# Performance work log

Hardware: AMD Instinct MI355X
Metric: run time of the kernel (lower is better)

Reference implementation:

```python
import jax, jax.numpy as jnp
import numpy as np

EPS = 1e-12  # F.normalize eps

def _unfold3(x):
    # x: [B,C,H,W] -> [B, C*9, H*W], matching F.unfold(kernel=3, padding=1)
    B, C, H, W = x.shape
    xp = jnp.pad(x, ((0, 0), (0, 0), (1, 1), (1, 1)))
    pats = jnp.stack([xp[:, :, i:i + H, j:j + W]
                      for i in range(3) for j in range(3)], axis=2)  # [B,C,9,H,W]
    return pats.reshape(B, C * 9, H * W)

def _fold3(t, H, W):
    # inverse of _unfold3 with overlap-add, matching F.fold(kernel=3, padding=1)
    B, CK, L = t.shape
    C = CK // 9
    t = t.reshape(B, C, 3, 3, H, W)
    out = jnp.zeros((B, C, H + 2, W + 2), t.dtype)
    for i in range(3):
        for j in range(3):
            out = out.at[:, :, i:i + H, j:j + W].add(t[:, :, i, j])
    return out[:, :, 1:1 + H, 1:1 + W]

def setup_inputs() -> dict:
    key = jax.random.key(0)
    kV, kK, kQ = jax.random.split(key, 3)
    B, C, H, W = 4, 64, 64, 64
    return {
        'V': jax.random.normal(kV, (B, C, H, W), dtype=jnp.float32),
        'K': jax.random.normal(kK, (B, C, H, W), dtype=jnp.float32),
        'Q': jax.random.normal(kQ, (B, C, H, W), dtype=jnp.float32),
    }

def reference(V, K, Q):
    B, C, H, W = Q.shape
    Qu = _unfold3(Q)  # [B, C9, L]
    Ku = _unfold3(K)  # [B, C9, L]
    # F.normalize along the feature (C*9) axis for both K (after permute dim=2) and Q (dim=1)
    Kn = Ku / jnp.maximum(jnp.linalg.norm(Ku, axis=1, keepdims=True), EPS)
    Qn = Qu / jnp.maximum(jnp.linalg.norm(Qu, axis=1, keepdims=True), EPS)
    # R[b,k,q] = <Kn[b,:,k], Qn[b,:,q]>  -> [B, L, L]
    R = jnp.einsum('bfk,bfq->bkq', Kn, Qn)
    S = jnp.max(R, axis=1)        # [B, L]
    arg = jnp.argmax(R, axis=1)   # [B, L] best key patch per query position
    Vu = _unfold3(V)              # [B, C9, L]
    idx = jnp.broadcast_to(arg[:, None, :], Vu.shape)
    T_unfold = jnp.take_along_axis(Vu, idx, axis=2)  # gather along patch dim
    T = _fold3(T_unfold, H, W) / 9.0                 # [B, C, H, W]
    S = S.reshape(B, 1, H, W)
    return (S, T)
```

## Files before the change

kernel.cpp:

```cpp
#include <hip/hip_runtime.h>
#include <math.h>

#define HW 4096

typedef short bf16x8 __attribute__((ext_vector_type(8)));
typedef float floatx4 __attribute__((ext_vector_type(4)));
typedef unsigned short u16x8 __attribute__((ext_vector_type(8)));

__device__ __forceinline__ unsigned short f2bf_rne(float x) {
    unsigned int u = __float_as_uint(x);
    unsigned int r = (u + 0x7FFFu + ((u >> 16) & 1u)) >> 16;
    return (unsigned short)r;
}
__device__ __forceinline__ float bf2f(unsigned short h) {
    return __uint_as_float(((unsigned int)h) << 16);
}

__device__ __forceinline__ void gload_lds16(const void* gptr, void* lptr) {
    auto g = (const __attribute__((address_space(1))) unsigned int*)(unsigned long long)(gptr);
    auto l = (__attribute__((address_space(3))) unsigned int*)(unsigned int)(unsigned long long)(lptr);
    __builtin_amdgcn_global_load_lds(g, l, 16, 0, 0);
}

__global__ __launch_bounds__(256)
void prep_kernel(const float* __restrict__ Q, const float* __restrict__ K,
                 const float* __restrict__ V,
                 unsigned short* __restrict__ Aq, unsigned short* __restrict__ Bq,
                 float* __restrict__ VT,
                 float* __restrict__ pix2q, float* __restrict__ pix2k) {
    __shared__ float sT[64][65];
    const int tid = threadIdx.x;
    const int p0 = blockIdx.x * 64;
    const int b = blockIdx.y;
    const int which = blockIdx.z;
    const float* __restrict__ src = (which == 0) ? Q : ((which == 1) ? K : V);

#pragma unroll
    for (int it = 0; it < 16; ++it) {
        int idx = it * 256 + tid;
        int c = idx >> 6, x = idx & 63;
        sT[c][x] = src[((size_t)b * 64 + c) * HW + p0 + x];
    }
    __syncthreads();
    const int pp = tid >> 2, qt = tid & 3;

    if (which == 2) {
        float* dst = VT + ((size_t)b * 4096 + p0 + pp) * 64 + qt * 16;
#pragma unroll
        for (int j = 0; j < 4; ++j) {
            float4 v = make_float4(sT[qt * 16 + 4 * j + 0][pp], sT[qt * 16 + 4 * j + 1][pp],
                                   sT[qt * 16 + 4 * j + 2][pp], sT[qt * 16 + 4 * j + 3][pp]);
            *(float4*)(dst + 4 * j) = v;
        }
        return;
    }

    const int isK = which;
    unsigned short* __restrict__ dst = isK ? Bq : Aq;
    float* __restrict__ pix2 = isK ? pix2k : pix2q;
    const size_t base = ((size_t)b * 4096 + p0 + pp) * 192;
    {
        float sq = 0.f;
        u16x8 hv[2], lv[2];
#pragma unroll
        for (int g = 0; g < 2; ++g)
#pragma unroll
            for (int j = 0; j < 8; ++j) {
                int c = qt * 16 + g * 8 + j;
                float x = sT[c][pp];
                sq = fmaf(x, x, sq);
                unsigned short h = f2bf_rne(x);
                hv[g][j] = h;
                lv[g][j] = f2bf_rne(x - bf2f(h));
            }
        sq += __shfl_xor(sq, 1, 64);
        sq += __shfl_xor(sq, 2, 64);
        if (qt == 0) pix2[(b << 12) + p0 + pp] = sq;
#pragma unroll
        for (int g = 0; g < 2; ++g) {
            int co = qt * 16 + g * 8;
            *(u16x8*)(dst + base + co)       = hv[g];
            *(u16x8*)(dst + base + 64 + co)  = isK ? lv[g] : hv[g];
            *(u16x8*)(dst + base + 128 + co) = isK ? hv[g] : lv[g];
        }
    }
}

__global__ void patchnorm_kernel(const float* __restrict__ pix2q, const float* __restrict__ pix2k,
                                 float* __restrict__ rnq, float* __restrict__ rnk) {
    int idx = blockIdx.x * 256 + threadIdx.x;
    int b = idx >> 12, p = idx & 4095;
    int py = p >> 6, px = p & 63;
    float sq = 0.f, sk = 0.f;
    for (int dy = -1; dy <= 1; ++dy)
        for (int dx = -1; dx <= 1; ++dx) {
            int yy = py + dy, xx = px + dx;
            if ((unsigned)yy < 64u && (unsigned)xx < 64u) {
                int o = (b << 12) + (yy << 6) + xx;
                sq += pix2q[o];
                sk += pix2k[o];
            }
        }
    rnq[idx] = 1.f / fmaxf(sqrtf(sq), 1e-12f);
    rnk[idx] = 1.f / fmaxf(sqrtf(sk), 1e-12f);
}

#define WAITV(n_) asm volatile("s_waitcnt vmcnt(" #n_ ")" ::: "memory")
#define PBAR(n_) do { WAITV(n_); __builtin_amdgcn_s_barrier(); \
                      asm volatile("" ::: "memory"); } while (0)

#define ISSUE_A(c_, sg_, slot_) do { \
    const char* g_ = Aqb + (size_t)(q0 - 64 + (c_) * 64) * 384 + (sg_) * 128; \
    gload_lds16(g_ + g0off, smem + (slot_) * 8192 + l0off); \
    gload_lds16(g_ + g1off, smem + (slot_) * 8192 + l1off); \
} while (0)
#define ISSUE_B(c_, sg_, slot_) do { \
    const char* g_ = Bqb + (size_t)(k0 - 64 + (c_) * 64) * 384 + (sg_) * 128; \
    gload_lds16(g_ + g0off, smemB + (slot_) * 8192 + l0off); \
    gload_lds16(g_ + g1off, smemB + (slot_) * 8192 + l1off); \
} while (0)

#define MM16(af_, bfr_) do { \
    __builtin_amdgcn_s_setprio(1); \
    _Pragma("unroll") \
    for (int mt = 0; mt < 4; ++mt) \
        _Pragma("unroll") \
        for (int nt = 0; nt < 4; ++nt) \
            acc[mt][nt] = __builtin_amdgcn_mfma_f32_16x16x32_bf16( \
                (af_)[mt], (bfr_)[nt], acc[mt][nt], 0, 0, 0); \
    __builtin_amdgcn_s_setprio(0); \
} while (0)

#define STEP_S0(D_) do { \
    const char* As_ = smem + (wm + (D_)) * 8192; \
    const char* Bs_ = smemB + (wn + (D_)) * 8192; \
    _Pragma("unroll") \
    for (int kk = 0; kk < 2; ++kk) { \
        const int pk_ = kk ? posK1 : posK0; \
        _Pragma("unroll") \
        for (int mt = 0; mt < 4; ++mt) \
            afc[kk][mt] = *(const bf16x8*)(As_ + mt * 2048 + rowB + pk_); \
        _Pragma("unroll") \
        for (int nt = 0; nt < 4; ++nt) \
            bfc[kk][nt] = *(const bf16x8*)(Bs_ + nt * 2048 + rowB + pk_); \
        MM16(afc[kk], bfc[kk]); \
    } \
} while (0)

#define STEP_S1(D_) do { \
    const int xb_ = wn + (D_); \
    const char* Bs_ = smemB + (xb_ < 2 ? xb_ + 3 : xb_ - 2) * 8192; \
    _Pragma("unroll") \
    for (int kk = 0; kk < 2; ++kk) { \
        const int pk_ = kk ? posK1 : posK0; \
        bf16x8 bfr[4]; \
        _Pragma("unroll") \
        for (int nt = 0; nt < 4; ++nt) \
            bfr[nt] = *(const bf16x8*)(Bs_ + nt * 2048 + rowB + pk_); \
        MM16(afc[kk], bfr); \
    } \
} while (0)

#define STEP_S2(D_) do { \
    const int xa_ = wm + (D_); \
    const char* As_ = smem + ((xa_ & 1) ? (xa_ >> 1) : 4) * 8192; \
    _Pragma("unroll") \
    for (int kk = 0; kk < 2; ++kk) { \
        const int pk_ = kk ? posK1 : posK0; \
        bf16x8 af[4]; \
        _Pragma("unroll") \
        for (int mt = 0; mt < 4; ++mt) \
            af[mt] = *(const bf16x8*)(As_ + mt * 2048 + rowB + pk_); \
        MM16(af, bfc[kk]); \
    } \
} while (0)

__global__ __launch_bounds__(256, 2)
void gemm_fused_kernel(const unsigned short* __restrict__ Aq, const unsigned short* __restrict__ Bq,
                       const float* __restrict__ rnkA,
                       float* __restrict__ part_val, int* __restrict__ part_arg) {
    __shared__ __align__(16) char smem[81920];
    char* const smemB = smem + 40960;
    const int tid = threadIdx.x;
    const int lane = tid & 63, wid = tid >> 6;
    const int m15 = lane & 15, quad = lane >> 4;
    const int wm = wid & 1, wn = wid >> 1;
    const int f = blockIdx.x + (blockIdx.y << 5);
    const int o = ((f & 7) << 7) + (f >> 3);
    const int kt = o & 31, qt = o >> 5;
    const int k0 = kt << 7;
    const int q0 = qt << 7;
    const int b = blockIdx.z;
    const char* Aqb = (const char*)(Aq + (size_t)b * 4096 * 192);
    const char* Bqb = (const char*)(Bq + (size_t)b * 4096 * 192);
    const bool aInt = (q0 >= 64) && (q0 <= 4096 - 192);
    const bool bInt = (k0 >= 64) && (k0 <= 4096 - 192);

    const int rr0 = tid >> 3, ps = tid & 7;
    const int g0off = rr0 * 384 + (ps ^ (rr0 & 7)) * 16;
    const int l0off = tid * 16;
    const int rr1 = (256 + tid) >> 3;
    const int g1off = rr1 * 384 + (ps ^ (rr1 & 7)) * 16;
    const int l1off = (256 + tid) * 16;
    const int rowB = m15 * 128;
    const int posK0 = (quad ^ (m15 & 7)) * 16;
    const int posK1 = ((4 + quad) ^ (m15 & 7)) * 16;

    floatx4 acc[4][4];
#pragma unroll
    for (int i = 0; i < 4; ++i)
#pragma unroll
        for (int j = 0; j < 4; ++j) acc[i][j] = (floatx4)0.f;

    bf16x8 afc[2][4];
    bf16x8 bfc[2][4];

    if (aInt && bInt) {
        ISSUE_A(0, 0, 0); ISSUE_A(1, 0, 1); ISSUE_B(0, 0, 0); ISSUE_B(1, 0, 1);
        ISSUE_A(2, 0, 2); ISSUE_B(2, 0, 2); ISSUE_A(3, 0, 3); ISSUE_B(0, 1, 3);
        ISSUE_B(1, 1, 4); ISSUE_A(0, 2, 4);
        PBAR(12);                                      STEP_S0(0);
        PBAR(2);  ISSUE_A(1, 2, 0); ISSUE_B(2, 1, 0); STEP_S1(0);
        PBAR(2);  ISSUE_B(3, 0, 3);                   STEP_S2(0);
        PBAR(14); ISSUE_A(2, 2, 4);                   STEP_S0(1);
        PBAR(4);  ISSUE_B(3, 1, 1);                   STEP_S1(1);
        PBAR(2);  ISSUE_A(3, 2, 1);                   STEP_S2(1);
        PBAR(6);                                      STEP_S0(2);
        PBAR(2);                                      STEP_S1(2);
        PBAR(0);                                      STEP_S2(2);
        __syncthreads();
    } else {
        for (int seg = 0; seg < 3; ++seg) {
            const char* abL = Aqb + (size_t)(q0 - 64) * 384 + seg * 128;
            const char* bbL = Bqb + (size_t)(k0 - 64) * 384 + seg * 128;
            if (aInt) {
#pragma unroll
                for (int it = 0; it < 8; ++it) {
                    int slot = it * 256 + tid;
                    int row = slot >> 3, pos = slot & 7;
                    int G = pos ^ (row & 7);
                    gload_lds16(abL + (size_t)row * 384 + G * 16, smem + slot * 16);
                }
            } else {
#pragma unroll
                for (int it = 0; it < 8; ++it) {
                    int slot = it * 256 + tid;
                    int row = slot >> 3, pos = slot & 7;
                    int G = pos ^ (row & 7);
                    uint4 v = make_uint4(0u, 0u, 0u, 0u);
                    if ((unsigned)(q0 - 64 + row) < 4096u)
                        v = *(const uint4*)(abL + (size_t)row * 384 + G * 16);
                    *(uint4*)(smem + slot * 16) = v;
                }
            }
            if (bInt) {
#pragma unroll
                for (int it = 0; it < 8; ++it) {
                    int slot = it * 256 + tid;
                    int row = slot >> 3, pos = slot & 7;
                    int G = pos ^ (row & 7);
                    gload_lds16(bbL + (size_t)row * 384 + G * 16, smemB + slot * 16);
                }
            } else {
#pragma unroll
                for (int it = 0; it < 8; ++it) {
                    int slot = it * 256 + tid;
                    int row = slot >> 3, pos = slot & 7;
                    int G = pos ^ (row & 7);
                    uint4 v = make_uint4(0u, 0u, 0u, 0u);
                    if ((unsigned)(k0 - 64 + row) < 4096u)
                        v = *(const uint4*)(bbL + (size_t)row * 384 + G * 16);
                    *(uint4*)(smemB + slot * 16) = v;
                }
            }
            __syncthreads();
            STEP_S0(0); STEP_S0(1); STEP_S0(2);
            __syncthreads();
        }
    }

    float* Csh = (float*)smem;
    float* bvs = (float*)(smem + 34816);
    int*   bas = (int*)(smem + 35840);
    const int q_l = tid & 63;
    const int qr = tid >> 6;
    const int c0 = qr * 32;
    const float4 zero4 = make_float4(0.f, 0.f, 0.f, 0.f);

#pragma unroll
    for (int h = 0; h < 2; ++h) {
        if (h) __syncthreads();
        if (wm == h) {
#pragma unroll
            for (int mt = 0; mt < 4; ++mt)
#pragma unroll
                for (int nt = 0; nt < 4; ++nt)
#pragma unroll
                    for (int j = 0; j < 4; ++j)
                        Csh[(mt * 16 + quad * 4 + j) * 133 + wn * 64 + nt * 16 + m15] =
                            acc[mt][nt][j];
        }
        __syncthreads();

        const bool qm = q_l > 0;
        const bool qp = q_l < 63;
        const float* rC = Csh + q_l * 133;
        const float* rM = Csh + (q_l - 1) * 133;
        const float* rP = Csh + (q_l + 1) * 133;
        float4 prevm = (qm && c0 > 0) ? *(const float4*)&rM[c0 - 4] : zero4;
        float4 rpj   = qp ? *(const float4*)&rP[c0] : zero4;
        float bv = -INFINITY;
        int ba = 0;
#pragma unroll
        for (int j = 0; j < 8; ++j) {
            int c = c0 + 4 * j;
            float4 cen = *(const float4*)&rC[c];
            float4 rm4 = qm ? *(const float4*)&rM[c] : zero4;
            float4 rp1 = (qp && (c + 4) < 128) ? *(const float4*)&rP[c + 4] : zero4;
            float4 o4;
            o4.x = cen.x + (((c & 63) != 0) ? prevm.w : 0.f) + rpj.y;
            o4.y = cen.y + rm4.x + rpj.z;
            o4.z = cen.z + rm4.y + rpj.w;
            o4.w = cen.w + rm4.z + ((((c + 3) & 63) != 63) ? rp1.x : 0.f);
            float4 rk = *(const float4*)&rnkA[(b << 12) + k0 + c];
            float v0 = o4.x * rk.x; if (v0 > bv) { bv = v0; ba = k0 + c + 0; }
            float v1 = o4.y * rk.y; if (v1 > bv) { bv = v1; ba = k0 + c + 1; }
            float v2 = o4.z * rk.z; if (v2 > bv) { bv = v2; ba = k0 + c + 2; }
            float v3 = o4.w * rk.w; if (v3 > bv) { bv = v3; ba = k0 + c + 3; }
            prevm = rm4;
            rpj = rp1;
        }
        bvs[(qr << 6) + q_l] = bv;
        bas[(qr << 6) + q_l] = ba;
        __syncthreads();
        if (tid < 64) {
            float v = bvs[tid];
            int a = bas[tid];
#pragma unroll
            for (int s = 1; s < 4; ++s) {
                float v2 = bvs[(s << 6) + tid];
                if (v2 > v) { v = v2; a = bas[(s << 6) + tid]; }
            }
            int q = q0 + h * 64 + tid;
            part_val[(((b << 5) + kt) << 12) + q] = v;
            part_arg[(((b << 5) + kt) << 12) + q] = a;
        }
    }
}

__global__ __launch_bounds__(256)
void argcombine_kernel(const float* __restrict__ part_val, const int* __restrict__ part_arg,
                       const float* __restrict__ rnqA,
                       float* __restrict__ S_out, int* __restrict__ argF) {
    __shared__ float rv[4][64];
    __shared__ int ra[4][64];
    const int tid = threadIdx.x;
    const int qi = tid & 63, sg = tid >> 6;
    const int q = blockIdx.x * 64 + qi;
    const int b = blockIdx.y;
    const int base = (b << 17) + q;
    float bv = -INFINITY; int ba = 0;
#pragma unroll
    for (int s8 = 0; s8 < 8; ++s8) {
        int s = sg * 8 + s8;
        float v = part_val[base + (s << 12)];
        int aa = part_arg[base + (s << 12)];
        if (v > bv) { bv = v; ba = aa; }
    }
    rv[sg][qi] = bv; ra[sg][qi] = ba;
    __syncthreads();
    if (tid < 64) {
        float v = rv[0][tid]; int a = ra[0][tid];
#pragma unroll
        for (int s = 1; s < 4; ++s) {
            float v2 = rv[s][tid];
            if (v2 > v) { v = v2; a = ra[s][tid]; }
        }
        int idx = (b << 12) + blockIdx.x * 64 + tid;
        S_out[idx] = v * rnqA[idx];
        argF[idx] = a;
    }
}

__global__ __launch_bounds__(256)
void gatherT_kernel(const float* __restrict__ VT, const int* __restrict__ argF,
                    float* __restrict__ T_out) {
    __shared__ int sArg[192];
    const int y = blockIdx.x, b = blockIdx.y, cg = blockIdx.z;
    const int tid = threadIdx.x;
    if (tid < 192) {
        int r = tid >> 6, x = tid & 63;
        int yy = y - 1 + r;
        sArg[tid] = ((unsigned)yy < 64u) ? argF[(b << 12) + (yy << 6) + x] : 0;
    }
    __syncthreads();

    const int x = tid >> 2, cq = tid & 3;
    const float* Vb = VT + (size_t)b * 4096 * 64 + cg * 16 + cq * 4;
    float ax = 0.f, ay = 0.f, az = 0.f, aw = 0.f;
#pragma unroll
    for (int t = 0; t < 9; ++t) {
        int dy = t / 3 - 1, dx = t % 3 - 1;
        int qy = y - dy, qx = x - dx;
        if ((unsigned)qy < 64u && (unsigned)qx < 64u) {
            int a = sArg[(1 - dy) * 64 + qx];
            int sy = (a >> 6) + dy, sx = (a & 63) + dx;
            if ((unsigned)sy < 64u && (unsigned)sx < 64u) {
                float4 v = *(const float4*)(Vb + (size_t)((sy << 6) + sx) * 64);
                ax += v.x; ay += v.y; az += v.z; aw += v.w;
            }
        }
    }
    float* Tb = T_out + ((size_t)b * 64 + cg * 16 + cq * 4) * HW + (y << 6) + x;
    Tb[0]          = ax * (1.f / 9.f);
    Tb[HW]         = ay * (1.f / 9.f);
    Tb[2 * HW]     = az * (1.f / 9.f);
    Tb[3 * HW]     = aw * (1.f / 9.f);
}

extern "C" void kernel_launch(void* const* d_in, const int* in_sizes, int n_in,
                              void* d_out, int out_size, void* d_ws, size_t ws_size,
                              hipStream_t stream) {
    const float* V = (const float*)d_in[0];
    const float* K = (const float*)d_in[1];
    const float* Q = (const float*)d_in[2];
    float* S_out = (float*)d_out;
    float* T_out = S_out + 4 * HW;

    char* ws = (char*)d_ws;
    float* pix2q = (float*)(ws + 0);
    float* pix2k = (float*)(ws + 65536);
    float* rnq   = (float*)(ws + 131072);
    float* rnk   = (float*)(ws + 196608);
    float* part_val = (float*)(ws + 262144);
    int*   argF  = (int*)(ws + 4456448);
    int*   part_arg = (int*)(ws + 8650752);
    float* VT    = (float*)(ws + 10747904);
    unsigned short* Aq = (unsigned short*)(ws + 17039360);
    unsigned short* Bq = (unsigned short*)(ws + 23330816);

    prep_kernel<<<dim3(64, 4, 3), 256, 0, stream>>>(Q, K, V, Aq, Bq, VT, pix2q, pix2k);
    patchnorm_kernel<<<64, 256, 0, stream>>>(pix2q, pix2k, rnq, rnk);
    gemm_fused_kernel<<<dim3(32, 32, 4), 256, 0, stream>>>(Aq, Bq, rnk, part_val, part_arg);
    argcombine_kernel<<<dim3(64, 4), 256, 0, stream>>>(part_val, part_arg, rnq, S_out, argF);
    gatherT_kernel<<<dim3(64, 4, 4), 256, 0, stream>>>(VT, argF, T_out);
}
```

Measured before the change: 191.8 us.

## Enlarge GEMM tile to 256x256 with 512 threads and split hi/lo operand buffers

The fused correlation GEMM now computes 256x256 output tiles per block with 8 waves, each holding a 128x64 accumulator. The prep kernel stores the hi and lo bf16 parts in separate places, and the GEMM loads them into distinct LDS regions through a 5-slot ring. Each dy step issues three MFMA passes (hi*hi, hi*lo, lo*hi). The larger tiles raise data reuse per loaded byte and halve the number of partial argmax results that argcombine has to merge. In exchange the kernel uses 160KB of LDS with one block per CU, carries more accumulator register pressure, and has a simpler pipeline with less overlap.

```diff
diff --git a/kernel.cpp b/kernel.cpp
--- a/kernel.cpp
+++ b/kernel.cpp
@@ -79,9 +79,8 @@
 #pragma unroll
         for (int g = 0; g < 2; ++g) {
             int co = qt * 16 + g * 8;
-            *(u16x8*)(dst + base + co)       = hv[g];
-            *(u16x8*)(dst + base + 64 + co)  = isK ? lv[g] : hv[g];
-            *(u16x8*)(dst + base + 128 + co) = isK ? hv[g] : lv[g];
+            *(u16x8*)(dst + base + co)                     = hv[g];
+            *(u16x8*)(dst + base + (isK ? 64 : 128) + co)  = lv[g];
         }
     }
 }
@@ -106,207 +105,169 @@
 }
 
 #define WAITV(n_) asm volatile("s_waitcnt vmcnt(" #n_ ")" ::: "memory")
-#define PBAR(n_) do { WAITV(n_); __builtin_amdgcn_s_barrier(); \
-                      asm volatile("" ::: "memory"); } while (0)
-
-#define ISSUE_A(c_, sg_, slot_) do { \
-    const char* g_ = Aqb + (size_t)(q0 - 64 + (c_) * 64) * 384 + (sg_) * 128; \
-    gload_lds16(g_ + g0off, smem + (slot_) * 8192 + l0off); \
-    gload_lds16(g_ + g1off, smem + (slot_) * 8192 + l1off); \
+#define SB do { __builtin_amdgcn_s_barrier(); asm volatile("" ::: "memory"); } while (0)
+
+#define AHB 0
+#define ALB 40960
+#define BHB 81920
+#define BLB 122880
+#define SLOT5(u_) ((u_) >= 5 ? (u_) - 5 : (u_))
+
+#define ISS4(c_) do { \
+    const size_t ro_ = (size_t)((c_) * 64 + rr) * 384; \
+    gload_lds16(agb + ro_ +   0 + G16, smem + AHB + ((c_) % 5) * 8192 + t16); \
+    gload_lds16(agb + ro_ + 256 + G16, smem + ALB + ((c_) % 5) * 8192 + t16); \
+    gload_lds16(bgb + ro_ +   0 + G16, smem + BHB + ((c_) % 5) * 8192 + t16); \
+    gload_lds16(bgb + ro_ + 128 + G16, smem + BLB + ((c_) % 5) * 8192 + t16); \
 } while (0)
-#define ISSUE_B(c_, sg_, slot_) do { \
-    const char* g_ = Bqb + (size_t)(k0 - 64 + (c_) * 64) * 384 + (sg_) * 128; \
-    gload_lds16(g_ + g0off, smemB + (slot_) * 8192 + l0off); \
-    gload_lds16(g_ + g1off, smemB + (slot_) * 8192 + l1off); \
+
+#define GISS4(c_) do { \
+    const size_t ro_ = (size_t)((c_) * 64 + rr) * 384; \
+    uint4 va_ = make_uint4(0u,0u,0u,0u), vl_ = va_, wh_ = va_, wl_ = va_; \
+    if ((unsigned)(arow + (c_) * 64 + rr) < 4096u) { \
+        va_ = *(const uint4*)(agb + ro_ + G16); \
+        vl_ = *(const uint4*)(agb + ro_ + 256 + G16); } \
+    if ((unsigned)(brow + (c_) * 64 + rr) < 4096u) { \
+        wh_ = *(const uint4*)(bgb + ro_ + G16); \
+        wl_ = *(const uint4*)(bgb + ro_ + 128 + G16); } \
+    *(uint4*)(smem + AHB + ((c_) % 5) * 8192 + t16) = va_; \
+    *(uint4*)(smem + ALB + ((c_) % 5) * 8192 + t16) = vl_; \
+    *(uint4*)(smem + BHB + ((c_) % 5) * 8192 + t16) = wh_; \
+    *(uint4*)(smem + BLB + ((c_) % 5) * 8192 + t16) = wl_; \
 } while (0)
 
-#define MM16(af_, bfr_) do { \
+#define MM32(af_, bf_) do { \
     __builtin_amdgcn_s_setprio(1); \
     _Pragma("unroll") \
-    for (int mt = 0; mt < 4; ++mt) \
+    for (int mt_ = 0; mt_ < 8; ++mt_) \
         _Pragma("unroll") \
-        for (int nt = 0; nt < 4; ++nt) \
-            acc[mt][nt] = __builtin_amdgcn_mfma_f32_16x16x32_bf16( \
-                (af_)[mt], (bfr_)[nt], acc[mt][nt], 0, 0, 0); \
+        for (int nt_ = 0; nt_ < 4; ++nt_) \
+            acc[mt_][nt_] = __builtin_amdgcn_mfma_f32_16x16x32_bf16( \
+                (af_)[mt_], (bf_)[nt_], acc[mt_][nt_], 0, 0, 0); \
     __builtin_amdgcn_s_setprio(0); \
 } while (0)
 
-#define STEP_S0(D_) do { \
-    const char* As_ = smem + (wm + (D_)) * 8192; \
-    const char* Bs_ = smemB + (wn + (D_)) * 8192; \
+#define DY_STEP(dy_) do { \
+    const int sa0_ = SLOT5(wm2 * 2 + (dy_)); \
+    const int sa1_ = SLOT5(wm2 * 2 + (dy_) + 1); \
+    const int sb_  = SLOT5(wn + (dy_)); \
+    const char* Ah0_ = smem + AHB + sa0_ * 8192 + m15 * 128; \
+    const char* Ah1_ = smem + AHB + sa1_ * 8192 + m15 * 128; \
+    const char* Al0_ = smem + ALB + sa0_ * 8192 + m15 * 128; \
+    const char* Al1_ = smem + ALB + sa1_ * 8192 + m15 * 128; \
+    const char* Bh_  = smem + BHB + sb_ * 8192 + m15 * 128; \
+    const char* Bl_  = smem + BLB + sb_ * 8192 + m15 * 128; \
     _Pragma("unroll") \
     for (int kk = 0; kk < 2; ++kk) { \
         const int pk_ = kk ? posK1 : posK0; \
+        bf16x8 afc[8], bfc[4], tf[8]; \
         _Pragma("unroll") \
-        for (int mt = 0; mt < 4; ++mt) \
-            afc[kk][mt] = *(const bf16x8*)(As_ + mt * 2048 + rowB + pk_); \
+        for (int mt = 0; mt < 8; ++mt) \
+            afc[mt] = *(const bf16x8*)((mt < 4 ? Ah0_ : Ah1_) + (mt & 3) * 2048 + pk_); \
         _Pragma("unroll") \
         for (int nt = 0; nt < 4; ++nt) \
-            bfc[kk][nt] = *(const bf16x8*)(Bs_ + nt * 2048 + rowB + pk_); \
-        MM16(afc[kk], bfc[kk]); \
+            bfc[nt] = *(const bf16x8*)(Bh_ + nt * 2048 + pk_); \
+        MM32(afc, bfc); \
+        _Pragma("unroll") \
+        for (int nt = 0; nt < 4; ++nt) \
+            tf[nt] = *(const bf16x8*)(Bl_ + nt * 2048 + pk_); \
+        MM32(afc, tf); \
+        _Pragma("unroll") \
+        for (int mt = 0; mt < 8; ++mt) \
+            tf[mt] = *(const bf16x8*)((mt < 4 ? Al0_ : Al1_) + (mt & 3) * 2048 + pk_); \
+        MM32(tf, bfc); \
     } \
 } while (0)
 
-#define STEP_S1(D_) do { \
-    const int xb_ = wn + (D_); \
-    const char* Bs_ = smemB + (xb_ < 2 ? xb_ + 3 : xb_ - 2) * 8192; \
-    _Pragma("unroll") \
-    for (int kk = 0; kk < 2; ++kk) { \
-        const int pk_ = kk ? posK1 : posK0; \
-        bf16x8 bfr[4]; \
-        _Pragma("unroll") \
-        for (int nt = 0; nt < 4; ++nt) \
-            bfr[nt] = *(const bf16x8*)(Bs_ + nt * 2048 + rowB + pk_); \
-        MM16(afc[kk], bfr); \
-    } \
-} while (0)
-
-#define STEP_S2(D_) do { \
-    const int xa_ = wm + (D_); \
-    const char* As_ = smem + ((xa_ & 1) ? (xa_ >> 1) : 4) * 8192; \
-    _Pragma("unroll") \
-    for (int kk = 0; kk < 2; ++kk) { \
-        const int pk_ = kk ? posK1 : posK0; \
-        bf16x8 af[4]; \
-        _Pragma("unroll") \
-        for (int mt = 0; mt < 4; ++mt) \
-            af[mt] = *(const bf16x8*)(As_ + mt * 2048 + rowB + pk_); \
-        MM16(af, bfc[kk]); \
-    } \
-} while (0)
-
-__global__ __launch_bounds__(256, 2)
+__global__ __launch_bounds__(512, 1)
 void gemm_fused_kernel(const unsigned short* __restrict__ Aq, const unsigned short* __restrict__ Bq,
                        const float* __restrict__ rnkA,
                        float* __restrict__ part_val, int* __restrict__ part_arg) {
-    __shared__ __align__(16) char smem[81920];
-    char* const smemB = smem + 40960;
+    __shared__ __align__(16) char smem[163840];
     const int tid = threadIdx.x;
     const int lane = tid & 63, wid = tid >> 6;
     const int m15 = lane & 15, quad = lane >> 4;
-    const int wm = wid & 1, wn = wid >> 1;
-    const int f = blockIdx.x + (blockIdx.y << 5);
-    const int o = ((f & 7) << 7) + (f >> 3);
-    const int kt = o & 31, qt = o >> 5;
-    const int k0 = kt << 7;
-    const int q0 = qt << 7;
-    const int b = blockIdx.z;
-    const char* Aqb = (const char*)(Aq + (size_t)b * 4096 * 192);
-    const char* Bqb = (const char*)(Bq + (size_t)b * 4096 * 192);
-    const bool aInt = (q0 >= 64) && (q0 <= 4096 - 192);
-    const bool bInt = (k0 >= 64) && (k0 <= 4096 - 192);
-
-    const int rr0 = tid >> 3, ps = tid & 7;
-    const int g0off = rr0 * 384 + (ps ^ (rr0 & 7)) * 16;
-    const int l0off = tid * 16;
-    const int rr1 = (256 + tid) >> 3;
-    const int g1off = rr1 * 384 + (ps ^ (rr1 & 7)) * 16;
-    const int l1off = (256 + tid) * 16;
-    const int rowB = m15 * 128;
+    const int wn = wid & 3, wm2 = wid >> 2;
+    const int f = blockIdx.x;
+    const int o = ((f & 7) << 5) + (f >> 3);
+    const int kt = o & 15, qt = o >> 4;
+    const int k0 = kt << 8, q0 = qt << 8;
+    const int b = blockIdx.y;
+    const int arow = q0 - 64, brow = k0 - 64;
+    const char* agb = (const char*)(Aq + (size_t)b * 4096 * 192) + (ptrdiff_t)arow * 384;
+    const char* bgb = (const char*)(Bq + (size_t)b * 4096 * 192) + (ptrdiff_t)brow * 384;
+    const bool aInt = (q0 >= 64) && (q0 + 320 <= 4096);
+    const bool bInt = (k0 >= 64) && (k0 + 320 <= 4096);
+
+    const int rr = tid >> 3;
+    const int G16 = ((tid & 7) ^ (rr & 7)) * 16;
+    const int t16 = tid * 16;
     const int posK0 = (quad ^ (m15 & 7)) * 16;
     const int posK1 = ((4 + quad) ^ (m15 & 7)) * 16;
 
-    floatx4 acc[4][4];
-#pragma unroll
-    for (int i = 0; i < 4; ++i)
+    floatx4 acc[8][4];
+#pragma unroll
+    for (int i = 0; i < 8; ++i)
 #pragma unroll
         for (int j = 0; j < 4; ++j) acc[i][j] = (floatx4)0.f;
 
-    bf16x8 afc[2][4];
-    bf16x8 bfc[2][4];
-
     if (aInt && bInt) {
-        ISSUE_A(0, 0, 0); ISSUE_A(1, 0, 1); ISSUE_B(0, 0, 0); ISSUE_B(1, 0, 1);
-        ISSUE_A(2, 0, 2); ISSUE_B(2, 0, 2); ISSUE_A(3, 0, 3); ISSUE_B(0, 1, 3);
-        ISSUE_B(1, 1, 4); ISSUE_A(0, 2, 4);
-        PBAR(12);                                      STEP_S0(0);
-        PBAR(2);  ISSUE_A(1, 2, 0); ISSUE_B(2, 1, 0); STEP_S1(0);
-        PBAR(2);  ISSUE_B(3, 0, 3);                   STEP_S2(0);
-        PBAR(14); ISSUE_A(2, 2, 4);                   STEP_S0(1);
-        PBAR(4);  ISSUE_B(3, 1, 1);                   STEP_S1(1);
-        PBAR(2);  ISSUE_A(3, 2, 1);                   STEP_S2(1);
-        PBAR(6);                                      STEP_S0(2);
-        PBAR(2);                                      STEP_S1(2);
-        PBAR(0);                                      STEP_S2(2);
+        ISS4(0); ISS4(1); ISS4(2); ISS4(3);
+        ISS4(4);
+        WAITV(4); SB;
+        DY_STEP(0);
+        SB;
+        ISS4(5);
+        WAITV(4); SB;
+        DY_STEP(1);
+        SB; WAITV(0); SB;
+        DY_STEP(2);
         __syncthreads();
     } else {
-        for (int seg = 0; seg < 3; ++seg) {
-            const char* abL = Aqb + (size_t)(q0 - 64) * 384 + seg * 128;
-            const char* bbL = Bqb + (size_t)(k0 - 64) * 384 + seg * 128;
-            if (aInt) {
-#pragma unroll
-                for (int it = 0; it < 8; ++it) {
-                    int slot = it * 256 + tid;
-                    int row = slot >> 3, pos = slot & 7;
-                    int G = pos ^ (row & 7);
-                    gload_lds16(abL + (size_t)row * 384 + G * 16, smem + slot * 16);
-                }
-            } else {
-#pragma unroll
-                for (int it = 0; it < 8; ++it) {
-                    int slot = it * 256 + tid;
-                    int row = slot >> 3, pos = slot & 7;
-                    int G = pos ^ (row & 7);
-                    uint4 v = make_uint4(0u, 0u, 0u, 0u);
-                    if ((unsigned)(q0 - 64 + row) < 4096u)
-                        v = *(const uint4*)(abL + (size_t)row * 384 + G * 16);
-                    *(uint4*)(smem + slot * 16) = v;
-                }
-            }
-            if (bInt) {
-#pragma unroll
-                for (int it = 0; it < 8; ++it) {
-                    int slot = it * 256 + tid;
-                    int row = slot >> 3, pos = slot & 7;
-                    int G = pos ^ (row & 7);
-                    gload_lds16(bbL + (size_t)row * 384 + G * 16, smemB + slot * 16);
-                }
-            } else {
-#pragma unroll
-                for (int it = 0; it < 8; ++it) {
-                    int slot = it * 256 + tid;
-                    int row = slot >> 3, pos = slot & 7;
-                    int G = pos ^ (row & 7);
-                    uint4 v = make_uint4(0u, 0u, 0u, 0u);
-                    if ((unsigned)(k0 - 64 + row) < 4096u)
-                        v = *(const uint4*)(bbL + (size_t)row * 384 + G * 16);
-                    *(uint4*)(smemB + slot * 16) = v;
-                }
-            }
-            __syncthreads();
-            STEP_S0(0); STEP_S0(1); STEP_S0(2);
-            __syncthreads();
-        }
+        GISS4(0); GISS4(1); GISS4(2); GISS4(3);
+        __syncthreads();
+        DY_STEP(0);
+        __syncthreads();
+        GISS4(4);
+        __syncthreads();
+        DY_STEP(1);
+        __syncthreads();
+        GISS4(5);
+        __syncthreads();
+        DY_STEP(2);
+        __syncthreads();
     }
 
     float* Csh = (float*)smem;
-    float* bvs = (float*)(smem + 34816);
-    int*   bas = (int*)(smem + 35840);
+    float* bvs = (float*)(smem + 66816);
+    int*   bas = (int*)(smem + 68864);
     const int q_l = tid & 63;
     const int qr = tid >> 6;
     const int c0 = qr * 32;
     const float4 zero4 = make_float4(0.f, 0.f, 0.f, 0.f);
 
 #pragma unroll
-    for (int h = 0; h < 2; ++h) {
+    for (int h = 0; h < 4; ++h) {
         if (h) __syncthreads();
-        if (wm == h) {
-#pragma unroll
-            for (int mt = 0; mt < 4; ++mt)
+        if (wm2 == (h >> 1)) {
+#pragma unroll
+            for (int mt2 = 0; mt2 < 4; ++mt2) {
+                const int mt = ((h & 1) << 2) + mt2;
 #pragma unroll
                 for (int nt = 0; nt < 4; ++nt)
 #pragma unroll
                     for (int j = 0; j < 4; ++j)
-                        Csh[(mt * 16 + quad * 4 + j) * 133 + wn * 64 + nt * 16 + m15] =
+                        Csh[(mt2 * 16 + quad * 4 + j) * 261 + (wn << 6) + nt * 16 + m15] =
                             acc[mt][nt][j];
+            }
         }
         __syncthreads();
 
         const bool qm = q_l > 0;
         const bool qp = q_l < 63;
-        const float* rC = Csh + q_l * 133;
-        const float* rM = Csh + (q_l - 1) * 133;
-        const float* rP = Csh + (q_l + 1) * 133;
+        const float* rC = Csh + q_l * 261;
+        const float* rM = Csh + (q_l - 1) * 261;
+        const float* rP = Csh + (q_l + 1) * 261;
         float4 prevm = (qm && c0 > 0) ? *(const float4*)&rM[c0 - 4] : zero4;
         float4 rpj   = qp ? *(const float4*)&rP[c0] : zero4;
         float bv = -INFINITY;
@@ -316,7 +277,7 @@
             int c = c0 + 4 * j;
             float4 cen = *(const float4*)&rC[c];
             float4 rm4 = qm ? *(const float4*)&rM[c] : zero4;
-            float4 rp1 = (qp && (c + 4) < 128) ? *(const float4*)&rP[c + 4] : zero4;
+            float4 rp1 = (qp && (c + 4) < 256) ? *(const float4*)&rP[c + 4] : zero4;
             float4 o4;
             o4.x = cen.x + (((c & 63) != 0) ? prevm.w : 0.f) + rpj.y;
             o4.y = cen.y + rm4.x + rpj.z;
@@ -337,13 +298,13 @@
             float v = bvs[tid];
             int a = bas[tid];
 #pragma unroll
-            for (int s = 1; s < 4; ++s) {
+            for (int s = 1; s < 8; ++s) {
                 float v2 = bvs[(s << 6) + tid];
                 if (v2 > v) { v = v2; a = bas[(s << 6) + tid]; }
             }
-            int q = q0 + h * 64 + tid;
-            part_val[(((b << 5) + kt) << 12) + q] = v;
-            part_arg[(((b << 5) + kt) << 12) + q] = a;
+            int q = q0 + (h << 6) + tid;
+            part_val[(((b << 4) + kt) << 12) + q] = v;
+            part_arg[(((b << 4) + kt) << 12) + q] = a;
         }
     }
 }
@@ -358,11 +319,11 @@
     const int qi = tid & 63, sg = tid >> 6;
     const int q = blockIdx.x * 64 + qi;
     const int b = blockIdx.y;
-    const int base = (b << 17) + q;
+    const int base = (b << 16) + q;
     float bv = -INFINITY; int ba = 0;
 #pragma unroll
-    for (int s8 = 0; s8 < 8; ++s8) {
-        int s = sg * 8 + s8;
+    for (int i = 0; i < 4; ++i) {
+        int s = sg * 4 + i;
         float v = part_val[base + (s << 12)];
         int aa = part_arg[base + (s << 12)];
         if (v > bv) { bv = v; ba = aa; }
@@ -441,7 +402,7 @@
 
     prep_kernel<<<dim3(64, 4, 3), 256, 0, stream>>>(Q, K, V, Aq, Bq, VT, pix2q, pix2k);
     patchnorm_kernel<<<64, 256, 0, stream>>>(pix2q, pix2k, rnq, rnk);
-    gemm_fused_kernel<<<dim3(32, 32, 4), 256, 0, stream>>>(Aq, Bq, rnk, part_val, part_arg);
+    gemm_fused_kernel<<<dim3(256, 4), 512, 0, stream>>>(Aq, Bq, rnk, part_val, part_arg);
     argcombine_kernel<<<dim3(64, 4), 256, 0, stream>>>(part_val, part_arg, rnq, S_out, argF);
     gatherT_kernel<<<dim3(64, 4, 4), 256, 0, stream>>>(VT, argF, T_out);
 }
```

After: 210.5 us. +9.8%, slower.

## Fuse patch-norm and arg-combine kernels into GEMM and gather stages

Applied to the files above, without the earlier changes.

Removes the separate patchnorm and argcombine launches. Each GEMM block now computes its 128 key inverse norms into LDS from pix2k, and the gather kernel reduces the 32 partial max/arg values itself, with one channel group also writing S using a query norm computed on the spot. Prep no longer writes the unused duplicate bf16 segment, and the edge path in the GEMM reads the hi/lo segments at the new offsets. This saves two launches and some global round trips, at the cost of redundant partial reductions across the three row reads and four channel-group blocks in the gather kernel.

```diff
diff --git a/kernel.cpp b/kernel.cpp
--- a/kernel.cpp
+++ b/kernel.cpp
@@ -79,30 +79,10 @@
 #pragma unroll
         for (int g = 0; g < 2; ++g) {
             int co = qt * 16 + g * 8;
-            *(u16x8*)(dst + base + co)       = hv[g];
-            *(u16x8*)(dst + base + 64 + co)  = isK ? lv[g] : hv[g];
-            *(u16x8*)(dst + base + 128 + co) = isK ? hv[g] : lv[g];
-        }
-    }
-}
-
-__global__ void patchnorm_kernel(const float* __restrict__ pix2q, const float* __restrict__ pix2k,
-                                 float* __restrict__ rnq, float* __restrict__ rnk) {
-    int idx = blockIdx.x * 256 + threadIdx.x;
-    int b = idx >> 12, p = idx & 4095;
-    int py = p >> 6, px = p & 63;
-    float sq = 0.f, sk = 0.f;
-    for (int dy = -1; dy <= 1; ++dy)
-        for (int dx = -1; dx <= 1; ++dx) {
-            int yy = py + dy, xx = px + dx;
-            if ((unsigned)yy < 64u && (unsigned)xx < 64u) {
-                int o = (b << 12) + (yy << 6) + xx;
-                sq += pix2q[o];
-                sk += pix2k[o];
-            }
-        }
-    rnq[idx] = 1.f / fmaxf(sqrtf(sq), 1e-12f);
-    rnk[idx] = 1.f / fmaxf(sqrtf(sk), 1e-12f);
+            *(u16x8*)(dst + base + co)                     = hv[g];
+            *(u16x8*)(dst + base + (isK ? 64 : 128) + co)  = lv[g];
+        }
+    }
 }
 
 #define WAITV(n_) asm volatile("s_waitcnt vmcnt(" #n_ ")" ::: "memory")
@@ -177,7 +157,7 @@
 
 __global__ __launch_bounds__(256, 2)
 void gemm_fused_kernel(const unsigned short* __restrict__ Aq, const unsigned short* __restrict__ Bq,
-                       const float* __restrict__ rnkA,
+                       const float* __restrict__ pix2k,
                        float* __restrict__ part_val, int* __restrict__ part_arg) {
     __shared__ __align__(16) char smem[81920];
     char* const smemB = smem + 40960;
@@ -231,8 +211,8 @@
         __syncthreads();
     } else {
         for (int seg = 0; seg < 3; ++seg) {
-            const char* abL = Aqb + (size_t)(q0 - 64) * 384 + seg * 128;
-            const char* bbL = Bqb + (size_t)(k0 - 64) * 384 + seg * 128;
+            const char* abL = Aqb + (size_t)(q0 - 64) * 384 + ((seg == 2) ? 256 : 0);
+            const char* bbL = Bqb + (size_t)(k0 - 64) * 384 + ((seg == 1) ? 128 : 0);
             if (aInt) {
 #pragma unroll
                 for (int it = 0; it < 8; ++it) {
@@ -282,6 +262,19 @@
     float* Csh = (float*)smem;
     float* bvs = (float*)(smem + 34816);
     int*   bas = (int*)(smem + 35840);
+    float* Lrnk = (float*)(smem + 36864);
+    if (tid < 128) {
+        int k = k0 + tid;
+        int py = k >> 6, px = k & 63;
+        float sk = 0.f;
+        for (int dy = -1; dy <= 1; ++dy)
+            for (int dx = -1; dx <= 1; ++dx) {
+                int yy = py + dy, xx = px + dx;
+                if ((unsigned)yy < 64u && (unsigned)xx < 64u)
+                    sk += pix2k[(b << 12) + (yy << 6) + xx];
+            }
+        Lrnk[tid] = 1.f / fmaxf(sqrtf(sk), 1e-12f);
+    }
     const int q_l = tid & 63;
     const int qr = tid >> 6;
     const int c0 = qr * 32;
@@ -322,7 +315,7 @@
             o4.y = cen.y + rm4.x + rpj.z;
             o4.z = cen.z + rm4.y + rpj.w;
             o4.w = cen.w + rm4.z + ((((c + 3) & 63) != 63) ? rp1.x : 0.f);
-            float4 rk = *(const float4*)&rnkA[(b << 12) + k0 + c];
+            float4 rk = *(const float4*)&Lrnk[c];
             float v0 = o4.x * rk.x; if (v0 > bv) { bv = v0; ba = k0 + c + 0; }
             float v1 = o4.y * rk.y; if (v1 > bv) { bv = v1; ba = k0 + c + 1; }
             float v2 = o4.z * rk.z; if (v2 > bv) { bv = v2; ba = k0 + c + 2; }
@@ -349,49 +342,40 @@
 }
 
 __global__ __launch_bounds__(256)
-void argcombine_kernel(const float* __restrict__ part_val, const int* __restrict__ part_arg,
-                       const float* __restrict__ rnqA,
-                       float* __restrict__ S_out, int* __restrict__ argF) {
-    __shared__ float rv[4][64];
-    __shared__ int ra[4][64];
-    const int tid = threadIdx.x;
-    const int qi = tid & 63, sg = tid >> 6;
-    const int q = blockIdx.x * 64 + qi;
-    const int b = blockIdx.y;
-    const int base = (b << 17) + q;
-    float bv = -INFINITY; int ba = 0;
-#pragma unroll
-    for (int s8 = 0; s8 < 8; ++s8) {
-        int s = sg * 8 + s8;
-        float v = part_val[base + (s << 12)];
-        int aa = part_arg[base + (s << 12)];
-        if (v > bv) { bv = v; ba = aa; }
-    }
-    rv[sg][qi] = bv; ra[sg][qi] = ba;
-    __syncthreads();
-    if (tid < 64) {
-        float v = rv[0][tid]; int a = ra[0][tid];
-#pragma unroll
-        for (int s = 1; s < 4; ++s) {
-            float v2 = rv[s][tid];
-            if (v2 > v) { v = v2; a = ra[s][tid]; }
-        }
-        int idx = (b << 12) + blockIdx.x * 64 + tid;
-        S_out[idx] = v * rnqA[idx];
-        argF[idx] = a;
-    }
-}
-
-__global__ __launch_bounds__(256)
-void gatherT_kernel(const float* __restrict__ VT, const int* __restrict__ argF,
-                    float* __restrict__ T_out) {
+void gatherT_kernel(const float* __restrict__ VT,
+                    const float* __restrict__ part_val, const int* __restrict__ part_arg,
+                    const float* __restrict__ pix2q,
+                    float* __restrict__ S_out, float* __restrict__ T_out) {
     __shared__ int sArg[192];
     const int y = blockIdx.x, b = blockIdx.y, cg = blockIdx.z;
     const int tid = threadIdx.x;
     if (tid < 192) {
         int r = tid >> 6, x = tid & 63;
         int yy = y - 1 + r;
-        sArg[tid] = ((unsigned)yy < 64u) ? argF[(b << 12) + (yy << 6) + x] : 0;
+        int a = 0;
+        if ((unsigned)yy < 64u) {
+            int base = (b << 17) + (yy << 6) + x;
+            float bv = -INFINITY; int ba = 0;
+#pragma unroll 8
+            for (int s = 0; s < 32; ++s) {
+                float v = part_val[base + (s << 12)];
+                int aa = part_arg[base + (s << 12)];
+                if (v > bv) { bv = v; ba = aa; }
+            }
+            a = ba;
+            if (r == 1 && cg == 0) {
+                float sq = 0.f;
+                for (int dy = -1; dy <= 1; ++dy)
+                    for (int dx = -1; dx <= 1; ++dx) {
+                        int y2 = yy + dy, x2 = x + dx;
+                        if ((unsigned)y2 < 64u && (unsigned)x2 < 64u)
+                            sq += pix2q[(b << 12) + (y2 << 6) + x2];
+                    }
+                S_out[(b << 12) + (yy << 6) + x] =
+                    bv * (1.f / fmaxf(sqrtf(sq), 1e-12f));
+            }
+        }
+        sArg[tid] = a;
     }
     __syncthreads();
 
@@ -430,18 +414,13 @@
     char* ws = (char*)d_ws;
     float* pix2q = (float*)(ws + 0);
     float* pix2k = (float*)(ws + 65536);
-    float* rnq   = (float*)(ws + 131072);
-    float* rnk   = (float*)(ws + 196608);
     float* part_val = (float*)(ws + 262144);
-    int*   argF  = (int*)(ws + 4456448);
     int*   part_arg = (int*)(ws + 8650752);
     float* VT    = (float*)(ws + 10747904);
     unsigned short* Aq = (unsigned short*)(ws + 17039360);
     unsigned short* Bq = (unsigned short*)(ws + 23330816);
 
     prep_kernel<<<dim3(64, 4, 3), 256, 0, stream>>>(Q, K, V, Aq, Bq, VT, pix2q, pix2k);
-    patchnorm_kernel<<<64, 256, 0, stream>>>(pix2q, pix2k, rnq, rnk);
-    gemm_fused_kernel<<<dim3(32, 32, 4), 256, 0, stream>>>(Aq, Bq, rnk, part_val, part_arg);
-    argcombine_kernel<<<dim3(64, 4), 256, 0, stream>>>(part_val, part_arg, rnq, S_out, argF);
-    gatherT_kernel<<<dim3(64, 4, 4), 256, 0, stream>>>(VT, argF, T_out);
-}
+    gemm_fused_kernel<<<dim3(32, 32, 4), 256, 0, stream>>>(Aq, Bq, pix2k, part_val, part_arg);
+    gatherT_kernel<<<dim3(64, 4, 4), 256, 0, stream>>>(VT, part_val, part_arg, pix2q, S_out, T_out);
+}
```

Result: slower. 199.5 us (+4.0%).
